# Kernel optimization log

Measured on AMD Instinct MI355X. Metric: run time of the kernel, lower is better.

The kernel has to match this reference:

```python
import jax, jax.numpy as jnp
import numpy as np

MEAN = np.array([0.485, 0.456, 0.406], np.float32).reshape(1, 3, 1, 1)
STD = np.array([0.229, 0.224, 0.225], np.float32).reshape(1, 3, 1, 1)
BN_EPS = 1e-5


def _srm_kernels():
    """Standard SRM 30-filter 5x5 high-pass bank (Fridrich) -> [30,1,5,5]."""
    ks = []
    Z = lambda: np.zeros((5, 5), np.float32)
    D8 = [(-1, 0), (-1, 1), (0, 1), (1, 1), (1, 0), (1, -1), (0, -1), (-1, -1)]
    for dy, dx in D8:  # 8 first-order
        k = Z(); k[2, 2] = -1.0; k[2 + dy, 2 + dx] = 1.0; ks.append(k)
    for dy, dx in D8[:4]:  # 4 second-order
        k = Z(); k[2, 2] = -2.0; k[2 + dy, 2 + dx] = 1.0; k[2 - dy, 2 - dx] = 1.0
        ks.append(k / 2.0)
    for dy, dx in D8:  # 8 third-order
        k = Z()
        k[2 - dy, 2 - dx] = -1.0; k[2, 2] = 3.0
        k[2 + dy, 2 + dx] = -3.0; k[2 + 2 * dy, 2 + 2 * dx] = 1.0
        ks.append(k / 3.0)
    sq3 = np.array([[-1, 2, -1], [2, -4, 2], [-1, 2, -1]], np.float32) / 4.0
    k = Z(); k[1:4, 1:4] = sq3; ks.append(k)  # SQUARE 3x3
    sq5 = np.array([[-1, 2, -2, 2, -1], [2, -6, 8, -6, 2], [-2, 8, -12, 8, -2],
                    [2, -6, 8, -6, 2], [-1, 2, -2, 2, -1]], np.float32) / 12.0
    ks.append(sq5)  # SQUARE 5x5
    e3 = np.array([[-1, 2, -1], [2, -4, 2], [0, 0, 0]], np.float32) / 4.0
    for r in range(4):  # 4 EDGE 3x3
        k = Z(); k[1:4, 1:4] = np.rot90(e3, r); ks.append(k)
    e5 = np.array([[-1, 2, -2, 2, -1], [2, -6, 8, -6, 2], [-2, 8, -12, 8, -2],
                   [0, 0, 0, 0, 0], [0, 0, 0, 0, 0]], np.float32) / 4.0
    for r in range(4):  # 4 EDGE 5x5
        ks.append(np.rot90(e5, r).copy())
    return np.stack(ks)[:, None]  # [30,1,5,5]

SRM_K = jnp.asarray(_srm_kernels())
GAUSS_K = jnp.asarray((np.outer([1, 4, 6, 4, 1], [1, 4, 6, 4, 1]) / 256.0)
                      .astype(np.float32))[None, None]  # [1,1,5,5]
CFA_K = jnp.asarray((np.array([[0, 1, 0], [1, 0, 1], [0, 1, 0]], np.float32) / 4.0))[None, None]


def conv2d(x, w, b=None):
    y = jax.lax.conv_general_dilated(x, w, (1, 1), 'SAME',
                                     dimension_numbers=('NCHW', 'OIHW', 'NCHW'))
    if b is not None:
        y = y + b[None, :, None, None]
    return y


def batchnorm(x, g, b, m, v):
    inv = jax.lax.rsqrt(v + BN_EPS)
    return (x - m[None, :, None, None]) * (g * inv)[None, :, None, None] + b[None, :, None, None]


def extract_features(x):
    """Batched PRNU(1) + SRM(30) + CFA(1) feature maps -> [B,32,H,W]."""
    img = jnp.clip(x * STD + MEAN, 0.0, 1.0)  # denormalize
    gray = (0.299 * img[:, 0] + 0.587 * img[:, 1] + 0.114 * img[:, 2])[:, None]  # [B,1,H,W]
    prnu = gray - conv2d(gray, GAUSS_K)            # denoise-subtract noise residual
    srm = conv2d(gray, SRM_K)                       # [B,30,H,W]
    green = img[:, 1:2]
    cfa = green - conv2d(green, CFA_K)              # CFA interpolation residual
    return jnp.concatenate([prnu, srm, cfa], axis=1)  # [B,32,H,W]


def setup_inputs() -> dict:
    key = jax.random.key(0)
    ks = jax.random.split(key, 16)
    B, H, W = 16, 256, 256
    d = {"x": jax.random.normal(ks[0], (B, 3, H, W), jnp.float32)}
    cins = [32, 64, 64, 64]
    for i in range(4):
        cin, co = cins[i], 64
        scale = (2.0 / (cin * 9)) ** 0.5  # kaiming
        d[f"w{i+1}"] = jax.random.normal(ks[1 + i], (co, cin, 3, 3), jnp.float32) * scale
        d[f"b{i+1}"] = jnp.zeros((co,), jnp.float32)
        d[f"g{i+1}"] = jnp.ones((co,), jnp.float32)
        d[f"be{i+1}"] = jnp.zeros((co,), jnp.float32)
        d[f"m{i+1}"] = jax.random.normal(ks[5 + i], (co,), jnp.float32) * 0.1
        d[f"v{i+1}"] = jax.random.uniform(ks[9 + i], (co,), jnp.float32, 0.5, 1.5)
    return d


def reference(x, w1, b1, g1, be1, m1, v1, w2, b2, g2, be2, m2, v2,
              w3, b3, g3, be3, m3, v3, w4, b4, g4, be4, m4, v4):
    h = extract_features(x)
    for w, b, g, be, m, v in ((w1, b1, g1, be1, m1, v1), (w2, b2, g2, be2, m2, v2),
                              (w3, b3, g3, be3, m3, v3), (w4, b4, g4, be4, m4, v4)):
        h = jax.nn.relu(batchnorm(conv2d(h, w, b), g, be, m, v))
    return h  # [B,64,H,W]
```

## Files before the change

### kernel.cpp

```cpp
#include <hip/hip_runtime.h>
#include <hip/hip_bf16.h>
#include <cstddef>

#define B_ 16
#define H_ 256
#define W_ 256
#define HW_ (H_ * W_)
#define P_ 258

typedef _Float16 half8 __attribute__((ext_vector_type(8)));
typedef float floatx4 __attribute__((ext_vector_type(4)));

__device__ __forceinline__ void gload_lds16(void* lds, const void* g) {
  __builtin_amdgcn_global_load_lds(
      (const __attribute__((address_space(1))) unsigned int*)g,
      (__attribute__((address_space(3))) unsigned int*)lds, 16, 0, 0);
}

template <int C>
__global__ __launch_bounds__(256) void zero_border(_Float16* __restrict__ buf) {
  int idx = blockIdx.x * 256 + threadIdx.x;
  int total = 16 * 1028 * (C / 8);
  if (idx >= total) return;
  int cg = idx % (C / 8);
  int rest = idx / (C / 8);
  int p = rest % 1028;
  int b = rest / 1028;
  int row, col;
  if (p < 258) { row = 0; col = p; }
  else if (p < 516) { row = 257; col = p - 258; }
  else if (p < 772) { row = p - 515; col = 0; }
  else { row = p - 771; col = 257; }
  *(floatx4*)&buf[(((size_t)b * P_ + row) * P_ + col) * C + cg * 8] = (floatx4)0.f;
}

__global__ __launch_bounds__(256) void feat_kernel(const float* __restrict__ x,
                                                   _Float16* __restrict__ F) {
  __shared__ float sg[36][37];
  __shared__ float sgr[36][37];

  const int b = blockIdx.z;
  const int y0 = blockIdx.y * 32;
  const int x0 = blockIdx.x * 32;
  const float* xb = x + (size_t)b * 3 * HW_;

  for (int i = threadIdx.x; i < 36 * 36; i += 256) {
    int iy = i / 36, ix = i % 36;
    int gy = y0 + iy - 2, gx = x0 + ix - 2;
    float gray = 0.f, green = 0.f;
    if (gy >= 0 && gy < H_ && gx >= 0 && gx < W_) {
      int idx = gy * W_ + gx;
      float r = fminf(fmaxf(xb[idx] * 0.229f + 0.485f, 0.f), 1.f);
      float g = fminf(fmaxf(xb[idx + HW_] * 0.224f + 0.456f, 0.f), 1.f);
      float bl = fminf(fmaxf(xb[idx + 2 * HW_] * 0.225f + 0.406f, 0.f), 1.f);
      gray = 0.299f * r + 0.587f * g + 0.114f * bl;
      green = g;
    }
    sg[iy][ix] = gray;
    sgr[iy][ix] = green;
  }
  __syncthreads();

  for (int p = threadIdx.x; p < 32 * 32; p += 256) {
    const int py = p >> 5, px = p & 31;
    const int ly = py + 2, lx = px + 2;
#define G(dy, dx) sg[ly + (dy)][lx + (dx)]
    float f[32];
    const float c = G(0, 0);

    {
      const float ga[5] = {1.f, 4.f, 6.f, 4.f, 1.f};
      float s = 0.f;
#pragma unroll
      for (int i = 0; i < 5; i++) {
        float rs = 0.f;
#pragma unroll
        for (int j = 0; j < 5; j++) rs += ga[j] * G(i - 2, j - 2);
        s += ga[i] * rs;
      }
      f[0] = c - s * (1.0f / 256.0f);
    }

    const int dy8[8] = {-1, -1, 0, 1, 1, 1, 0, -1};
    const int dx8[8] = {0, 1, 1, 1, 0, -1, -1, -1};

#pragma unroll
    for (int k = 0; k < 8; k++) f[1 + k] = G(dy8[k], dx8[k]) - c;
#pragma unroll
    for (int k = 0; k < 4; k++)
      f[9 + k] = 0.5f * (G(dy8[k], dx8[k]) + G(-dy8[k], -dx8[k])) - c;
#pragma unroll
    for (int k = 0; k < 8; k++)
      f[13 + k] = (-G(-dy8[k], -dx8[k]) + 3.f * c - 3.f * G(dy8[k], dx8[k]) +
                   G(2 * dy8[k], 2 * dx8[k])) * (1.f / 3.f);

    {
      const float sq3[3][3] = {{-1, 2, -1}, {2, -4, 2}, {-1, 2, -1}};
      float s = 0.f;
#pragma unroll
      for (int i = 0; i < 3; i++)
#pragma unroll
        for (int j = 0; j < 3; j++) s += sq3[i][j] * G(i - 1, j - 1);
      f[21] = s * 0.25f;
    }
    {
      const float sq5[5][5] = {{-1, 2, -2, 2, -1},
                               {2, -6, 8, -6, 2},
                               {-2, 8, -12, 8, -2},
                               {2, -6, 8, -6, 2},
                               {-1, 2, -2, 2, -1}};
      float s = 0.f;
#pragma unroll
      for (int i = 0; i < 5; i++)
#pragma unroll
        for (int j = 0; j < 5; j++) s += sq5[i][j] * G(i - 2, j - 2);
      f[22] = s * (1.0f / 12.0f);
    }
    {
      const float e3[3][3] = {{-1, 2, -1}, {2, -4, 2}, {0, 0, 0}};
      float s0 = 0.f, s1 = 0.f, s2 = 0.f, s3 = 0.f;
#pragma unroll
      for (int i = 0; i < 3; i++)
#pragma unroll
        for (int j = 0; j < 3; j++) {
          float v = G(i - 1, j - 1);
          s0 += e3[i][j] * v;
          s1 += e3[j][2 - i] * v;
          s2 += e3[2 - i][2 - j] * v;
          s3 += e3[2 - j][i] * v;
        }
      f[23] = s0 * 0.25f;
      f[24] = s1 * 0.25f;
      f[25] = s2 * 0.25f;
      f[26] = s3 * 0.25f;
    }
    {
      const float e5[5][5] = {{-1, 2, -2, 2, -1},
                              {2, -6, 8, -6, 2},
                              {-2, 8, -12, 8, -2},
                              {0, 0, 0, 0, 0},
                              {0, 0, 0, 0, 0}};
      float s0 = 0.f, s1 = 0.f, s2 = 0.f, s3 = 0.f;
#pragma unroll
      for (int i = 0; i < 5; i++)
#pragma unroll
        for (int j = 0; j < 5; j++) {
          float v = G(i - 2, j - 2);
          s0 += e5[i][j] * v;
          s1 += e5[j][4 - i] * v;
          s2 += e5[4 - i][4 - j] * v;
          s3 += e5[4 - j][i] * v;
        }
      f[27] = s0 * 0.25f;
      f[28] = s1 * 0.25f;
      f[29] = s2 * 0.25f;
      f[30] = s3 * 0.25f;
    }
    {
      float gc = sgr[ly][lx];
      f[31] = gc - 0.25f * (sgr[ly - 1][lx] + sgr[ly][lx - 1] +
                            sgr[ly][lx + 1] + sgr[ly + 1][lx]);
    }
#undef G

    _Float16 h[32];
#pragma unroll
    for (int cc = 0; cc < 32; cc++) h[cc] = (_Float16)f[cc];
    floatx4* dst =
        (floatx4*)&F[(((size_t)b * P_ + (y0 + py + 1)) * P_ + (x0 + px + 1)) * 32];
    const floatx4* src = (const floatx4*)h;
#pragma unroll
    for (int k = 0; k < 4; k++) dst[k] = src[k];
  }
}

__global__ void wprep_kernel(const float* __restrict__ w,
                             const float* __restrict__ bias,
                             const float* __restrict__ g,
                             const float* __restrict__ be,
                             const float* __restrict__ m,
                             const float* __restrict__ v,
                             _Float16* __restrict__ wp,
                             float* __restrict__ sc, float* __restrict__ sh,
                             int cin) {
  int i = blockIdx.x * 256 + threadIdx.x;
  int total = cin * 9 * 64;
  if (i < total) {
    int j = i & 7;
    int co = (i >> 3) & 63;
    int rest = i >> 9;
    int t = rest % 9;
    int qc = rest / 9;
    int ci = qc * 8 + j;
    wp[i] = (_Float16)w[((size_t)co * cin + ci) * 9 + t];
  }
  if (i < 64) {
    float s = g[i] * rsqrtf(v[i] + 1e-5f);
    sc[i] = s;
    sh[i] = be[i] + (bias[i] - m[i]) * s;
  }
}

template <int CIN, bool FINAL>
__global__ __launch_bounds__(256, 2) void conv_mfma(
    const _Float16* __restrict__ in, const _Float16* __restrict__ wp,
    const float* __restrict__ sc, const float* __restrict__ sh,
    void* __restrict__ outv) {
  __shared__ char smem[42240 + 36864];
  _Float16(*s_in)[10][66][8] = (_Float16(*)[10][66][8])smem;
  _Float16(*s_w)[9][64][8] = (_Float16(*)[9][64][8])(smem + 42240);

  const int tid = threadIdx.x;
  const int b = blockIdx.z;
  const int y0 = blockIdx.y * 8;
  const int x0 = blockIdx.x * 64;
  const int wid = tid >> 6;
  const int lane = tid & 63;
  const int quad = lane >> 4;
  const int ln = lane & 15;

  floatx4 acc[8][4];
#pragma unroll
  for (int mt = 0; mt < 8; mt++)
#pragma unroll
    for (int nt = 0; nt < 4; nt++) acc[mt][nt] = (floatx4)0.f;

  for (int kc = 0; kc < CIN / 32; kc++) {
    __syncthreads();
    for (int i = tid; i < 2640; i += 256) {
      int q = i / 660, rem = i % 660;
      int row = rem / 66, col = rem % 66;
      gload_lds16(smem + i * 16,
                  &in[(((size_t)b * P_ + (y0 + row)) * P_ + (x0 + col)) * CIN +
                      kc * 32 + q * 8]);
    }
    for (int i = tid; i < 2304; i += 256) {
      gload_lds16(smem + 42240 + i * 16, wp + ((size_t)kc * 2304 + i) * 8);
    }
    __syncthreads();

#pragma unroll
    for (int t = 0; t < 9; t++) {
      const int ty = t / 3, tx = t % 3;
      half8 a[8], bb[4];
#pragma unroll
      for (int nt = 0; nt < 4; nt++)
        bb[nt] = *(const half8*)&s_w[quad][t][nt * 16 + ln][0];
#pragma unroll
      for (int mt = 0; mt < 8; mt++)
        a[mt] = *(const half8*)
            &s_in[quad][2 * wid + ty + (mt >> 2)][(mt & 3) * 16 + ln + tx][0];
#pragma unroll
      for (int mt = 0; mt < 8; mt++)
#pragma unroll
        for (int nt = 0; nt < 4; nt++)
          acc[mt][nt] = __builtin_amdgcn_mfma_f32_16x16x32_f16(
              a[mt], bb[nt], acc[mt][nt], 0, 0, 0);
    }
  }

  if (FINAL) {
    float* out = (float*)outv;
#pragma unroll
    for (int nt = 0; nt < 4; nt++) {
      int co = nt * 16 + ln;
      float s = sc[co], t0 = sh[co];
#pragma unroll
      for (int mt = 0; mt < 8; mt++) {
        int y = y0 + 2 * wid + (mt >> 2);
        int xb = x0 + (mt & 3) * 16 + quad * 4;
        floatx4 vv;
#pragma unroll
        for (int r = 0; r < 4; r++) vv[r] = fmaxf(acc[mt][nt][r] * s + t0, 0.f);
        *(floatx4*)&out[(((size_t)b * 64 + co) * H_ + y) * W_ + xb] = vv;
      }
    }
  } else {
    __syncthreads();
    _Float16* s_out = (_Float16*)smem + wid * 8192;
#pragma unroll
    for (int nt = 0; nt < 4; nt++) {
      int co = nt * 16 + ln;
      float s = sc[co], t0 = sh[co];
#pragma unroll
      for (int mt = 0; mt < 8; mt++) {
        int base = ((mt >> 2) * 64 + (mt & 3) * 16 + quad * 4) * 64 + co;
#pragma unroll
        for (int r = 0; r < 4; r++)
          s_out[base + r * 64] = (_Float16)fmaxf(acc[mt][nt][r] * s + t0, 0.f);
      }
    }
    _Float16* out = (_Float16*)outv;
#pragma unroll
    for (int k = 0; k < 16; k++) {
      int u = k * 64 + lane;
      int cog = u & 7, px = (u >> 3) & 63, rw = u >> 9;
      int gy = y0 + 2 * wid + rw + 1, gx = x0 + px + 1;
      *(floatx4*)&out[(((size_t)b * P_ + gy) * P_ + gx) * 64 + cog * 8] =
          *(const floatx4*)&s_out[u * 8];
    }
  }
}

extern "C" void kernel_launch(void* const* d_in, const int* in_sizes, int n_in,
                              void* d_out, int out_size, void* d_ws,
                              size_t ws_size, hipStream_t stream) {
  const float* x = (const float*)d_in[0];
#define LAYER_PTRS(i)                                                       \
  const float* w##i = (const float*)d_in[1 + ((i)-1) * 6 + 0];              \
  const float* b##i = (const float*)d_in[1 + ((i)-1) * 6 + 1];              \
  const float* g##i = (const float*)d_in[1 + ((i)-1) * 6 + 2];              \
  const float* be##i = (const float*)d_in[1 + ((i)-1) * 6 + 3];             \
  const float* m##i = (const float*)d_in[1 + ((i)-1) * 6 + 4];              \
  const float* v##i = (const float*)d_in[1 + ((i)-1) * 6 + 5];
  LAYER_PTRS(1)
  LAYER_PTRS(2)
  LAYER_PTRS(3)
  LAYER_PTRS(4)
#undef LAYER_PTRS

  char* ws = (char*)d_ws;
  const size_t featB = (size_t)16 * P_ * P_ * 32 * 2;
  const size_t actB64 = (size_t)16 * P_ * P_ * 64 * 2;
  _Float16* feat = (_Float16*)ws;
  _Float16* actA = (_Float16*)(ws + featB);
  _Float16* actB = (_Float16*)(ws + featB + actB64);
  char* wbase = ws + featB + 2 * actB64;
  _Float16* wp1 = (_Float16*)(wbase);
  _Float16* wp2 = (_Float16*)(wbase + 36864);
  _Float16* wp3 = (_Float16*)(wbase + 36864 + 73728);
  _Float16* wp4 = (_Float16*)(wbase + 36864 + 2 * 73728);
  float* scsh = (float*)(wbase + 36864 + 3 * 73728);
  float *sc1 = scsh, *sh1 = scsh + 64;
  float *sc2 = scsh + 128, *sh2 = scsh + 192;
  float *sc3 = scsh + 256, *sh3 = scsh + 320;
  float *sc4 = scsh + 384, *sh4 = scsh + 448;

  wprep_kernel<<<72, 256, 0, stream>>>(w1, b1, g1, be1, m1, v1, wp1, sc1, sh1, 32);
  wprep_kernel<<<144, 256, 0, stream>>>(w2, b2, g2, be2, m2, v2, wp2, sc2, sh2, 64);
  wprep_kernel<<<144, 256, 0, stream>>>(w3, b3, g3, be3, m3, v3, wp3, sc3, sh3, 64);
  wprep_kernel<<<144, 256, 0, stream>>>(w4, b4, g4, be4, m4, v4, wp4, sc4, sh4, 64);

  zero_border<32><<<257, 256, 0, stream>>>(feat);
  zero_border<64><<<514, 256, 0, stream>>>(actA);
  zero_border<64><<<514, 256, 0, stream>>>(actB);

  dim3 fgrid(W_ / 32, H_ / 32, B_);
  feat_kernel<<<fgrid, 256, 0, stream>>>(x, feat);

  dim3 cgrid(W_ / 64, H_ / 8, B_);
  conv_mfma<32, false><<<cgrid, 256, 0, stream>>>(feat, wp1, sc1, sh1, actA);
  conv_mfma<64, false><<<cgrid, 256, 0, stream>>>(actA, wp2, sc2, sh2, actB);
  conv_mfma<64, false><<<cgrid, 256, 0, stream>>>(actB, wp3, sc3, sh3, actA);
  conv_mfma<64, true><<<cgrid, 256, 0, stream>>>(actA, wp4, sc4, sh4, d_out);
}
```

Before: 720.9 us.

## Switch intermediate activations to channel-group-blocked layout with swizzled LDS staging

Intermediate fp16 activation buffers move from pixel-major NHWC with 32/64 interleaved channels to a blocked [B][C/8][H][W][8] layout. Each 16-byte global-to-LDS load for a channel group now reads contiguous pixels, which improves coalescing of the conv input fetch. The epilogue LDS staging buffer gains an XOR swizzle on channel groups to avoid bank conflicts, and its store loop now writes one channel group per row across lanes. The border-zeroing and feature kernels are updated to match. Writes from feat_kernel become strided across four planes, and each channel group's rows are now far apart in memory.

```diff
diff --git a/kernel.cpp b/kernel.cpp
--- a/kernel.cpp
+++ b/kernel.cpp
@@ -8,6 +8,7 @@
 #define HW_ (H_ * W_)
 #define P_ 258
 
+
 typedef _Float16 half8 __attribute__((ext_vector_type(8)));
 typedef float floatx4 __attribute__((ext_vector_type(4)));
 
@@ -17,21 +18,22 @@
       (__attribute__((address_space(3))) unsigned int*)lds, 16, 0, 0);
 }
 
-template <int C>
+template <int NCG>
 __global__ __launch_bounds__(256) void zero_border(_Float16* __restrict__ buf) {
   int idx = blockIdx.x * 256 + threadIdx.x;
-  int total = 16 * 1028 * (C / 8);
+  int total = 16 * NCG * 1028;
   if (idx >= total) return;
-  int cg = idx % (C / 8);
-  int rest = idx / (C / 8);
-  int p = rest % 1028;
-  int b = rest / 1028;
+  int p = idx % 1028;
+  int rest = idx / 1028;
+  int cg = rest % NCG;
+  int b = rest / NCG;
   int row, col;
   if (p < 258) { row = 0; col = p; }
   else if (p < 516) { row = 257; col = p - 258; }
   else if (p < 772) { row = p - 515; col = 0; }
   else { row = p - 771; col = 257; }
-  *(floatx4*)&buf[(((size_t)b * P_ + row) * P_ + col) * C + cg * 8] = (floatx4)0.f;
+  *(floatx4*)&buf[(((size_t)(b * NCG + cg) * P_ + row) * P_ + col) * 8] =
+      (floatx4)0.f;
 }
 
 __global__ __launch_bounds__(256) void feat_kernel(const float* __restrict__ x,
@@ -166,11 +168,11 @@
     _Float16 h[32];
 #pragma unroll
     for (int cc = 0; cc < 32; cc++) h[cc] = (_Float16)f[cc];
-    floatx4* dst =
-        (floatx4*)&F[(((size_t)b * P_ + (y0 + py + 1)) * P_ + (x0 + px + 1)) * 32];
     const floatx4* src = (const floatx4*)h;
 #pragma unroll
-    for (int k = 0; k < 4; k++) dst[k] = src[k];
+    for (int cg = 0; cg < 4; cg++)
+      *(floatx4*)&F[(((size_t)(b * 4 + cg) * P_ + (y0 + py + 1)) * P_ +
+                     (x0 + px + 1)) * 8] = src[cg];
   }
 }
 
@@ -231,8 +233,8 @@
       int q = i / 660, rem = i % 660;
       int row = rem / 66, col = rem % 66;
       gload_lds16(smem + i * 16,
-                  &in[(((size_t)b * P_ + (y0 + row)) * P_ + (x0 + col)) * CIN +
-                      kc * 32 + q * 8]);
+                  &in[(((size_t)(b * (CIN / 8) + kc * 4 + q) * P_ +
+                        (y0 + row)) * P_ + (x0 + col)) * 8]);
     }
     for (int i = tid; i < 2304; i += 256) {
       gload_lds16(smem + 42240 + i * 16, wp + ((size_t)kc * 2304 + i) * 8);
@@ -282,22 +284,26 @@
     for (int nt = 0; nt < 4; nt++) {
       int co = nt * 16 + ln;
       float s = sc[co], t0 = sh[co];
+      int cog = co >> 3, clo = co & 7;
 #pragma unroll
       for (int mt = 0; mt < 8; mt++) {
-        int base = ((mt >> 2) * 64 + (mt & 3) * 16 + quad * 4) * 64 + co;
-#pragma unroll
-        for (int r = 0; r < 4; r++)
-          s_out[base + r * 64] = (_Float16)fmaxf(acc[mt][nt][r] * s + t0, 0.f);
+        int pix0 = (mt >> 2) * 64 + (mt & 3) * 16 + quad * 4;
+#pragma unroll
+        for (int r = 0; r < 4; r++) {
+          int pix = pix0 + r;
+          s_out[pix * 64 + (((cog ^ (pix & 7)) << 3) | clo)] =
+              (_Float16)fmaxf(acc[mt][nt][r] * s + t0, 0.f);
+        }
       }
     }
     _Float16* out = (_Float16*)outv;
 #pragma unroll
     for (int k = 0; k < 16; k++) {
-      int u = k * 64 + lane;
-      int cog = u & 7, px = (u >> 3) & 63, rw = u >> 9;
-      int gy = y0 + 2 * wid + rw + 1, gx = x0 + px + 1;
-      *(floatx4*)&out[(((size_t)b * P_ + gy) * P_ + gx) * 64 + cog * 8] =
-          *(const floatx4*)&s_out[u * 8];
+      int rw = k >> 3, cog = k & 7;
+      int pix = rw * 64 + lane;
+      int gy = y0 + 2 * wid + rw + 1, gx = x0 + lane + 1;
+      *(floatx4*)&out[(((size_t)(b * 8 + cog) * P_ + gy) * P_ + gx) * 8] =
+          *(const floatx4*)&s_out[pix * 64 + ((cog ^ (lane & 7)) << 3)];
     }
   }
 }
@@ -320,8 +326,8 @@
 #undef LAYER_PTRS
 
   char* ws = (char*)d_ws;
-  const size_t featB = (size_t)16 * P_ * P_ * 32 * 2;
-  const size_t actB64 = (size_t)16 * P_ * P_ * 64 * 2;
+  const size_t featB = (size_t)16 * 4 * P_ * P_ * 8 * 2;
+  const size_t actB64 = (size_t)16 * 8 * P_ * P_ * 8 * 2;
   _Float16* feat = (_Float16*)ws;
   _Float16* actA = (_Float16*)(ws + featB);
   _Float16* actB = (_Float16*)(ws + featB + actB64);
@@ -341,9 +347,9 @@
   wprep_kernel<<<144, 256, 0, stream>>>(w3, b3, g3, be3, m3, v3, wp3, sc3, sh3, 64);
   wprep_kernel<<<144, 256, 0, stream>>>(w4, b4, g4, be4, m4, v4, wp4, sc4, sh4, 64);
 
-  zero_border<32><<<257, 256, 0, stream>>>(feat);
-  zero_border<64><<<514, 256, 0, stream>>>(actA);
-  zero_border<64><<<514, 256, 0, stream>>>(actB);
+  zero_border<4><<<257, 256, 0, stream>>>(feat);
+  zero_border<8><<<514, 256, 0, stream>>>(actA);
+  zero_border<8><<<514, 256, 0, stream>>>(actB);
 
   dim3 fgrid(W_ / 32, H_ / 32, B_);
   feat_kernel<<<fgrid, 256, 0, stream>>>(x, feat);
```

Measured after the change: 643.7 us. 10.7% less time.
